# Performance work log

Measured on AMD Instinct MI355X. Metric: run time of the kernel, lower is better.

## Reference

```python
import jax, jax.numpy as jnp
import numpy as np

D_MODEL = 1024
H = 16
D_K = D_MODEL // H


def setup_inputs() -> dict:
    key = jax.random.key(0)
    ks = jax.random.split(key, 7)
    B, S = 4, 2048
    scale = 1.0 / np.sqrt(D_MODEL)
    return {
        "q": jax.random.normal(ks[0], (B, S, D_MODEL), dtype=jnp.float32),
        "k": jax.random.normal(ks[1], (B, S, D_MODEL), dtype=jnp.float32),
        "v": jax.random.normal(ks[2], (B, S, D_MODEL), dtype=jnp.float32),
        "W_q": jax.random.normal(ks[3], (D_MODEL, D_MODEL), dtype=jnp.float32) * scale,
        "W_k": jax.random.normal(ks[4], (D_MODEL, D_MODEL), dtype=jnp.float32) * scale,
        "W_v": jax.random.normal(ks[5], (D_MODEL, D_MODEL), dtype=jnp.float32) * scale,
        "W_o": jax.random.normal(ks[6], (D_MODEL, D_MODEL), dtype=jnp.float32) * scale,
    }


def reference(q, k, v, W_q, W_k, W_v, W_o):
    B, S, _ = q.shape
    # nn.Linear(bias=False): y = x @ W.T
    def proj(x, W):
        return (x @ W.T).reshape(B, -1, H, D_K).transpose(0, 2, 1, 3)  # [B,H,S,d_k]
    Q = proj(q, W_q)
    K = proj(k, W_k)
    V = proj(v, W_v)
    scores = jnp.einsum('bhqd,bhkd->bhqk', Q, K) / jnp.sqrt(jnp.float32(D_K))
    attn = jax.nn.softmax(scores, axis=-1)  # dropout p=0.0 -> identity
    ctx = jnp.einsum('bhqk,bhkd->bhqd', attn, V)
    ctx = ctx.transpose(0, 2, 1, 3).reshape(B, S, H * D_K)
    return ctx @ W_o.T
```

## Files before the change

### kernel.cpp

```cpp
#include <hip/hip_runtime.h>
#include <stdint.h>


typedef __attribute__((ext_vector_type(8))) short bf16x8;
typedef __attribute__((ext_vector_type(4))) float f32x4;

__device__ __forceinline__ void lds_async16(const void* g, void* l) {
  __builtin_amdgcn_global_load_lds(
      (const __attribute__((address_space(1))) void*)g,
      (__attribute__((address_space(3))) void*)l, 16, 0, 0);
}

__device__ __forceinline__ unsigned short f2bf(float f) {
  union { float f; unsigned u; } v; v.f = f;
  unsigned u = v.u + 0x7fffu + ((v.u >> 16) & 1u);
  return (unsigned short)(u >> 16);
}

__device__ __forceinline__ float fast_exp2(float x) {
#if __has_builtin(__builtin_amdgcn_exp2f)
  return __builtin_amdgcn_exp2f(x);
#else
  return exp2f(x);
#endif
}

__device__ __forceinline__ unsigned pk2(float a, float b) {
#if __has_builtin(__builtin_amdgcn_cvt_pk_bf16_f32)
  typedef __bf16 bf16v2 __attribute__((ext_vector_type(2)));
  union { bf16v2 v; unsigned u; } x;
  x.v = __builtin_amdgcn_cvt_pk_bf16_f32(a, b);
  return x.u;
#else
  return (unsigned)f2bf(a) | ((unsigned)f2bf(b) << 16);
#endif
}

__global__ void cvt_kernel(const float* s0, const float* s1, const float* s2, const float* s3,
                           unsigned short* d0, unsigned short* d1, unsigned short* d2, unsigned short* d3,
                           int n4) {
  int which = blockIdx.y;
  const float* s = which == 0 ? s0 : which == 1 ? s1 : which == 2 ? s2 : s3;
  unsigned short* d = which == 0 ? d0 : which == 1 ? d1 : which == 2 ? d2 : d3;
  int i = blockIdx.x * 256 + threadIdx.x;
  if (i < n4) {
    float4 v = ((const float4*)s)[i];
    ushort4 o;
    o.x = f2bf(v.x); o.y = f2bf(v.y); o.z = f2bf(v.z); o.w = f2bf(v.w);
    ((ushort4*)d)[i] = o;
  }
}

struct G256 { f32x4 acc[4][4]; };

__device__ __forceinline__ void stage_half(const unsigned short* __restrict__ src,
                                           int rowbase, int kt, int h,
                                           unsigned short* lds, int tid) {
  const int srow = tid >> 3;
  const int g = tid & 7;
  const int col = ((g ^ (srow & 7)) << 3);
  const unsigned short* s0 = src + (size_t)(rowbase + h * 128 + srow) * 1024 + kt * 64 + col;
  char* d0 = (char*)lds + h * 16384 + tid * 16;
  lds_async16(s0, d0);
  lds_async16(s0 + (size_t)64 * 1024, d0 + 8192);
}

__device__ __forceinline__ void read2(const unsigned short* buf, int rowbase, int c16, int q4,
                                      int tbase, bf16x8 (&fr)[2][2]) {
#pragma unroll
  for (int tt = 0; tt < 2; ++tt)
#pragma unroll
    for (int ks = 0; ks < 2; ++ks) {
      int row = rowbase + (tbase + tt) * 16 + c16;
      fr[tt][ks] = *(const bf16x8*)(buf + row * 64 + (((ks * 4 + q4) ^ (row & 7)) * 8));
    }
}

__device__ __forceinline__ void mfma_quad(G256& G, const bf16x8 (&af)[2][2],
                                          const bf16x8 (&bf)[2][2], int i0, int j0) {
  __builtin_amdgcn_s_setprio(1);
#pragma unroll
  for (int ii = 0; ii < 2; ++ii)
#pragma unroll
    for (int jj = 0; jj < 2; ++jj)
#pragma unroll
      for (int ks = 0; ks < 2; ++ks)
        G.acc[i0 + ii][j0 + jj] = __builtin_amdgcn_mfma_f32_16x16x32_bf16(
            af[ii][ks], bf[jj][ks], G.acc[i0 + ii][j0 + jj], 0, 0, 0);
  __builtin_amdgcn_s_setprio(0);
}

__device__ __forceinline__ void gemm256_core(const unsigned short* __restrict__ A,
                                             const unsigned short* __restrict__ B,
                                             int tm, int tn,
                                             unsigned short* As, unsigned short* Bs,
                                             G256& G) {
  const int tid = threadIdx.x;
  const int lane = tid & 63;
  const int wv = tid >> 6;
  const int wm = wv & 1, wn = wv >> 1;
  const int c16 = lane & 15, q4 = lane >> 4;
  const int am = tm * 128, bn = tn * 256;
  const int arow = wm * 64, brow = wn * 64;

#pragma unroll
  for (int i = 0; i < 4; ++i)
#pragma unroll
    for (int j = 0; j < 4; ++j)
#pragma unroll
      for (int r = 0; r < 4; ++r) G.acc[i][j][r] = 0.f;

  stage_half(A, am, 0, 0, As + 0 * 8192, tid);
  stage_half(B, bn, 0, 0, Bs + 0 * 16384, tid);
  stage_half(B, bn, 0, 1, Bs + 0 * 16384, tid);
  stage_half(A, am, 1, 0, As + 1 * 8192, tid);
  stage_half(B, bn, 1, 0, Bs + 1 * 16384, tid);
  stage_half(B, bn, 1, 1, Bs + 1 * 16384, tid);

  bf16x8 af[2][2], bfa[2][2], bfb[2][2];

#pragma unroll
  for (int t = 0; t < 16; ++t) {
    const int bt = t % 3;
    const int b2 = (t + 2) % 3;
    const unsigned short* Ab = As + bt * 8192;
    const unsigned short* Bb = Bs + bt * 16384;
    if (t < 15) { asm volatile("s_waitcnt vmcnt(6)" ::: "memory"); }
    else        { asm volatile("s_waitcnt vmcnt(0)" ::: "memory"); }
    __builtin_amdgcn_s_barrier();
    if (t < 14) {
      stage_half(A, am, t + 2, 0, As + b2 * 8192, tid);
      stage_half(B, bn, t + 2, 0, Bs + b2 * 16384, tid);
      stage_half(B, bn, t + 2, 1, Bs + b2 * 16384, tid);
    }
    read2(Ab, arow, c16, q4, 0, af);
    read2(Bb, brow, c16, q4, 0, bfa);
    read2(Bb, brow, c16, q4, 2, bfb);
    mfma_quad(G, af, bfa, 0, 0);
    mfma_quad(G, af, bfb, 0, 2);
    __builtin_amdgcn_s_barrier();
    read2(Ab, arow, c16, q4, 2, af);
    mfma_quad(G, af, bfb, 2, 2);
    mfma_quad(G, af, bfa, 2, 0);
  }
}

__global__ __launch_bounds__(512, 1)
void qkv_kernel(const unsigned short* __restrict__ qb, const unsigned short* __restrict__ kb,
                const unsigned short* __restrict__ vb,
                const unsigned short* __restrict__ wq, const unsigned short* __restrict__ wk,
                const unsigned short* __restrict__ wv_,
                unsigned short* __restrict__ Qb, unsigned short* __restrict__ Kb,
                unsigned short* __restrict__ Vtb) {
  __shared__ unsigned short As[3 * 128 * 64];
  __shared__ unsigned short Bs[3 * 256 * 64];
  const int z = blockIdx.z;
  const unsigned short* A;
  const unsigned short* B;
  int tm, tn;
  if (z == 0)      { A = qb;  B = wq;  tm = blockIdx.y; tn = blockIdx.x; }
  else if (z == 1) { A = kb;  B = wk;  tm = blockIdx.y; tn = blockIdx.x; }
  else {
    A = wv_; B = vb;
    int idx = blockIdx.y * 4 + blockIdx.x;
    tm = idx >> 5;
    tn = idx & 31;
  }

  G256 G;
  gemm256_core(A, B, tm, tn, As, Bs, G);

  const int lane = threadIdx.x & 63;
  const int wv = threadIdx.x >> 6;
  const int wm = wv & 1, wn = wv >> 1;
  const int c16 = lane & 15, q4 = lane >> 4;
  const float qscale = 0.125f * 1.44269504f;

#pragma unroll
  for (int i = 0; i < 4; ++i)
#pragma unroll
    for (int j = 0; j < 4; ++j)
#pragma unroll
      for (int r = 0; r < 4; ++r) {
        int m = tm * 128 + wm * 64 + i * 16 + q4 * 4 + r;
        int n = tn * 256 + wn * 64 + j * 16 + c16;
        float val = G.acc[i][j][r];
        if (z < 2) {
          if (z == 0) val *= qscale;
          int b = m >> 11, s_ = m & 2047, h = n >> 6, d = n & 63;
          unsigned short* dst = z == 0 ? Qb : Kb;
          dst[(((size_t)(b * 16 + h) * 2048 + s_) << 6) | d] = f2bf(val);
        } else {
          int h = m >> 6, d = m & 63, b = n >> 11, s_ = n & 2047;
          int sl = s_ & 127;
          int sp = (sl & ~31) | (((sl >> 2) & 3) << 3) | (((sl >> 4) & 1) << 2) | (sl & 3);
          s_ = (s_ & ~127) | sp;
          Vtb[((size_t)((b * 16 + h) * 64 + d) << 11) | s_] = f2bf(val);
        }
      }
}

__global__ __launch_bounds__(512, 1)
void out_gemm(const unsigned short* __restrict__ A, const unsigned short* __restrict__ B,
              float* __restrict__ C) {
  __shared__ unsigned short As[3 * 128 * 64];
  __shared__ unsigned short Bs[3 * 256 * 64];
  G256 G;
  gemm256_core(A, B, blockIdx.y, blockIdx.x, As, Bs, G);
  const int lane = threadIdx.x & 63;
  const int wv = threadIdx.x >> 6;
  const int wm = wv & 1, wn = wv >> 1;
  const int c16 = lane & 15, q4 = lane >> 4;
#pragma unroll
  for (int i = 0; i < 4; ++i)
#pragma unroll
    for (int j = 0; j < 4; ++j)
#pragma unroll
      for (int r = 0; r < 4; ++r) {
        int m = blockIdx.y * 128 + wm * 64 + i * 16 + q4 * 4 + r;
        int n = blockIdx.x * 256 + wn * 64 + j * 16 + c16;
        C[(size_t)m * 1024 + n] = G.acc[i][j][r];
      }
}

__global__ __launch_bounds__(128, 2)
void attn_kernel(const unsigned short* __restrict__ Q,
                 const unsigned short* __restrict__ K,
                 const unsigned short* __restrict__ Vt,
                 unsigned short* __restrict__ ctx) {
  __shared__ unsigned short Ks[2][64 * 64];
  __shared__ unsigned short Vs[2][64 * 64];

  const int tid = threadIdx.x, lane = tid & 63, w = tid >> 6;
  const int c16 = lane & 15, q4 = lane >> 4;
  const int wbase = w * 64;
  const unsigned wgid = blockIdx.x;
  const int bh = (int)((wgid & 7u) * 8 + ((wgid >> 3) & 7u));
  const int qt = (int)(wgid >> 6);
  const unsigned short* Qp = Q + ((size_t)bh * 2048 + qt * 128) * 64;
  const unsigned short* Kp = K + (size_t)bh * 2048 * 64;
  const unsigned short* Vp = Vt + (size_t)bh * 64 * 2048;

  const int srow = tid >> 3;
  const int gcol = (((tid & 7) ^ (srow & 7)) << 3);

  {
    const unsigned short* Qr = Qp + (size_t)srow * 64 + gcol;
    char* base = (char*)Ks + tid * 16;
#pragma unroll
    for (int c = 0; c < 8; ++c) lds_async16(Qr + c * 16 * 64, base + c * 2048);
  }
  __syncthreads();
  const unsigned short* Kflat = &Ks[0][0];
  bf16x8 qf[4][2];
#pragma unroll
  for (int nn = 0; nn < 4; ++nn)
#pragma unroll
    for (int ks = 0; ks < 2; ++ks) {
      int qr = wbase + nn * 16 + c16;
      int pos = (ks * 4 + q4) ^ (qr & 7);
      qf[nn][ks] = *(const bf16x8*)(Kflat + qr * 64 + pos * 8);
    }
  __syncthreads();

  bf16x8 onesf;
  {
    short v = (c16 == 0) ? (short)0x3F80 : (short)0;
#pragma unroll
    for (int j = 0; j < 8; ++j) onesf[j] = v;
  }

  f32x4 oacc[4][4];
  f32x4 lacc[4];
#pragma unroll
  for (int nn = 0; nn < 4; ++nn) {
#pragma unroll
    for (int r = 0; r < 4; ++r) lacc[nn][r] = 0.f;
#pragma unroll
    for (int dj = 0; dj < 4; ++dj)
#pragma unroll
      for (int r = 0; r < 4; ++r) oacc[nn][dj][r] = 0.f;
  }

  const unsigned short* Kr0 = Kp + (size_t)srow * 64 + gcol;
  const unsigned short* Vr0 = Vp + (size_t)srow * 2048 + gcol;

  {
    char* kb = (char*)Ks[0] + tid * 16;
    char* vb = (char*)Vs[0] + tid * 16;
#pragma unroll
    for (int c = 0; c < 4; ++c) {
      lds_async16(Kr0 + (size_t)c * 16 * 64, kb + c * 2048);
      lds_async16(Vr0 + (size_t)c * 16 * 2048, vb + c * 2048);
    }
  }

  int cur = 0;
#pragma unroll 2
  for (int kt = 0; kt < 32; ++kt) {
    __syncthreads();
    if (kt < 31) {
      char* kb = (char*)Ks[cur ^ 1] + tid * 16;
      char* vb = (char*)Vs[cur ^ 1] + tid * 16;
      const unsigned short* Krn = Kr0 + (size_t)(kt + 1) * 64 * 64;
      const unsigned short* Vrn = Vr0 + (size_t)(kt + 1) * 64;
#pragma unroll
      for (int c = 0; c < 4; ++c) {
        lds_async16(Krn + (size_t)c * 16 * 64, kb + c * 2048);
        lds_async16(Vrn + (size_t)c * 16 * 2048, vb + c * 2048);
      }
    }

    const unsigned short* KsC = Ks[cur];
    const unsigned short* VsC = Vs[cur];

    bf16x8 kf[2][2][2];
#pragma unroll
    for (int c = 0; c < 2; ++c)
#pragma unroll
      for (int ms = 0; ms < 2; ++ms) {
        const int row = (c * 2 + ms) * 16 + c16;
        kf[c][ms][0] = *(const bf16x8*)(KsC + row * 64 + ((0 + q4) ^ (row & 7)) * 8);
        kf[c][ms][1] = *(const bf16x8*)(KsC + row * 64 + ((4 + q4) ^ (row & 7)) * 8);
      }
    bf16x8 vf0[4];
#pragma unroll
    for (int dj = 0; dj < 4; ++dj) {
      const int dr = dj * 16 + c16;
      vf0[dj] = *(const bf16x8*)(VsC + dr * 64 + ((q4 ^ (dr & 7))) * 8);
    }

    f32x4 s0[2][4], s1[2][4];
    __builtin_amdgcn_s_setprio(1);
#pragma unroll
    for (int ms = 0; ms < 2; ++ms)
#pragma unroll
      for (int nn = 0; nn < 4; ++nn) {
        f32x4 z = {0.f, 0.f, 0.f, 0.f};
        z = __builtin_amdgcn_mfma_f32_16x16x32_bf16(kf[0][ms][0], qf[nn][0], z, 0, 0, 0);
        z = __builtin_amdgcn_mfma_f32_16x16x32_bf16(kf[0][ms][1], qf[nn][1], z, 0, 0, 0);
        s0[ms][nn] = z;
      }
    __builtin_amdgcn_s_setprio(0);
    bf16x8 vf1[4];
#pragma unroll
    for (int dj = 0; dj < 4; ++dj) {
      const int dr = dj * 16 + c16;
      vf1[dj] = *(const bf16x8*)(VsC + dr * 64 + (((4 + q4) ^ (dr & 7))) * 8);
    }
    __builtin_amdgcn_s_setprio(1);
#pragma unroll
    for (int ms = 0; ms < 2; ++ms)
#pragma unroll
      for (int nn = 0; nn < 4; ++nn) {
        f32x4 z = {0.f, 0.f, 0.f, 0.f};
        z = __builtin_amdgcn_mfma_f32_16x16x32_bf16(kf[1][ms][0], qf[nn][0], z, 0, 0, 0);
        z = __builtin_amdgcn_mfma_f32_16x16x32_bf16(kf[1][ms][1], qf[nn][1], z, 0, 0, 0);
        s1[ms][nn] = z;
      }
    __builtin_amdgcn_s_setprio(0);

    {
      bf16x8 pfv[4];
#pragma unroll
      for (int nn = 0; nn < 4; ++nn) {
        union PU { unsigned u[4]; bf16x8 v; } pf;
        pf.u[0] = pk2(fast_exp2(s0[0][nn][0]), fast_exp2(s0[0][nn][1]));
        pf.u[1] = pk2(fast_exp2(s0[0][nn][2]), fast_exp2(s0[0][nn][3]));
        pf.u[2] = pk2(fast_exp2(s0[1][nn][0]), fast_exp2(s0[1][nn][1]));
        pf.u[3] = pk2(fast_exp2(s0[1][nn][2]), fast_exp2(s0[1][nn][3]));
        pfv[nn] = pf.v;
      }
      __builtin_amdgcn_s_setprio(1);
#pragma unroll
      for (int nn = 0; nn < 4; ++nn)
        lacc[nn] = __builtin_amdgcn_mfma_f32_16x16x32_bf16(pfv[nn], onesf, lacc[nn], 0, 0, 0);
#pragma unroll
      for (int dj = 0; dj < 4; ++dj)
#pragma unroll
        for (int nn = 0; nn < 4; ++nn)
          oacc[nn][dj] = __builtin_amdgcn_mfma_f32_16x16x32_bf16(pfv[nn], vf0[dj], oacc[nn][dj], 0, 0, 0);
      __builtin_amdgcn_s_setprio(0);
    }
    {
      bf16x8 pfv[4];
#pragma unroll
      for (int nn = 0; nn < 4; ++nn) {
        union PU { unsigned u[4]; bf16x8 v; } pf;
        pf.u[0] = pk2(fast_exp2(s1[0][nn][0]), fast_exp2(s1[0][nn][1]));
        pf.u[1] = pk2(fast_exp2(s1[0][nn][2]), fast_exp2(s1[0][nn][3]));
        pf.u[2] = pk2(fast_exp2(s1[1][nn][0]), fast_exp2(s1[1][nn][1]));
        pf.u[3] = pk2(fast_exp2(s1[1][nn][2]), fast_exp2(s1[1][nn][3]));
        pfv[nn] = pf.v;
      }
      __builtin_amdgcn_s_setprio(1);
#pragma unroll
      for (int nn = 0; nn < 4; ++nn)
        lacc[nn] = __builtin_amdgcn_mfma_f32_16x16x32_bf16(pfv[nn], onesf, lacc[nn], 0, 0, 0);
#pragma unroll
      for (int dj = 0; dj < 4; ++dj)
#pragma unroll
        for (int nn = 0; nn < 4; ++nn)
          oacc[nn][dj] = __builtin_amdgcn_mfma_f32_16x16x32_bf16(pfv[nn], vf1[dj], oacc[nn][dj], 0, 0, 0);
      __builtin_amdgcn_s_setprio(0);
    }
    cur ^= 1;
  }

  int b = bh >> 4, h = bh & 15;
#pragma unroll
  for (int nn = 0; nn < 4; ++nn)
#pragma unroll
    for (int r = 0; r < 4; ++r) {
      float l = __shfl(lacc[nn][r], lane & 48, 64);
      float inv = 1.f / l;
      int s_ = qt * 128 + wbase + nn * 16 + q4 * 4 + r;
#pragma unroll
      for (int dj = 0; dj < 4; ++dj) {
        int d = dj * 16 + c16;
        ctx[((size_t)(b * 2048 + s_)) * 1024 + h * 64 + d] = f2bf(oacc[nn][dj][r] * inv);
      }
    }
}

extern "C" void kernel_launch(void* const* d_in, const int* in_sizes, int n_in,
                              void* d_out, int out_size, void* d_ws, size_t ws_size,
                              hipStream_t stream) {
  const float* q  = (const float*)d_in[0];
  const float* k  = (const float*)d_in[1];
  const float* v  = (const float*)d_in[2];
  const float* Wq = (const float*)d_in[3];
  const float* Wk = (const float*)d_in[4];
  const float* Wv = (const float*)d_in[5];
  const float* Wo = (const float*)d_in[6];

  char* ws = (char*)d_ws;
  unsigned short* qb  = (unsigned short*)(ws);
  unsigned short* kb  = (unsigned short*)(ws + (16u << 20));
  unsigned short* vb  = (unsigned short*)(ws + (32u << 20));
  unsigned short* wqb = (unsigned short*)(ws + (48u << 20));
  unsigned short* wkb = (unsigned short*)(ws + (50u << 20));
  unsigned short* wvb = (unsigned short*)(ws + (52u << 20));
  unsigned short* wob = (unsigned short*)(ws + (54u << 20));
  unsigned short* Qb  = (unsigned short*)(ws + (56u << 20));
  unsigned short* Kb  = (unsigned short*)(ws + (72u << 20));
  unsigned short* Vtb = (unsigned short*)(ws + (88u << 20));
  unsigned short* ctxb = qb;

  cvt_kernel<<<dim3(1024, 4), 256, 0, stream>>>(Wq, Wk, Wv, Wo, wqb, wkb, wvb, wob, 262144);
  cvt_kernel<<<dim3(8192, 3), 256, 0, stream>>>(q, k, v, q, qb, kb, vb, qb, 2097152);

  qkv_kernel<<<dim3(4, 64, 3), 512, 0, stream>>>(qb, kb, vb, wqb, wkb, wvb, Qb, Kb, Vtb);

  attn_kernel<<<dim3(1024), 128, 0, stream>>>(Qb, Kb, Vtb, ctxb);

  out_gemm<<<dim3(4, 64), 512, 0, stream>>>(ctxb, wob, (float*)d_out);
}
```

Before: 322.2 us.

## Fuse fp32-to-bf16 conversion into GEMM loaders, dropping separate cvt kernels

Removes the two standalone conversion kernels and has the QKV and output GEMMs load fp32 operands straight into registers, convert them to bf16 and write them to LDS, with a register-staged software pipeline. This saves a full extra read and write of the activations and weights plus two launches. In exchange the GEMMs read twice as many bytes per tile, lose asynchronous global-to-LDS loads for fp32 operands, and add conversion ALU work and register pressure. Weights are now re-read and re-converted by every tile that uses them.

```diff
diff --git a/kernel.cpp b/kernel.cpp
--- a/kernel.cpp
+++ b/kernel.cpp
@@ -36,33 +36,56 @@
 #endif
 }
 
-__global__ void cvt_kernel(const float* s0, const float* s1, const float* s2, const float* s3,
-                           unsigned short* d0, unsigned short* d1, unsigned short* d2, unsigned short* d3,
-                           int n4) {
-  int which = blockIdx.y;
-  const float* s = which == 0 ? s0 : which == 1 ? s1 : which == 2 ? s2 : s3;
-  unsigned short* d = which == 0 ? d0 : which == 1 ? d1 : which == 2 ? d2 : d3;
-  int i = blockIdx.x * 256 + threadIdx.x;
-  if (i < n4) {
-    float4 v = ((const float4*)s)[i];
-    ushort4 o;
-    o.x = f2bf(v.x); o.y = f2bf(v.y); o.z = f2bf(v.z); o.w = f2bf(v.w);
-    ((ushort4*)d)[i] = o;
-  }
-}
-
 struct G256 { f32x4 acc[4][4]; };
 
-__device__ __forceinline__ void stage_half(const unsigned short* __restrict__ src,
-                                           int rowbase, int kt, int h,
-                                           unsigned short* lds, int tid) {
+__device__ __forceinline__ void stage_lds_unit(const unsigned short* __restrict__ src,
+                                               int rowbase, int kt, int halves,
+                                               unsigned short* lds, int tid) {
   const int srow = tid >> 3;
-  const int g = tid & 7;
-  const int col = ((g ^ (srow & 7)) << 3);
-  const unsigned short* s0 = src + (size_t)(rowbase + h * 128 + srow) * 1024 + kt * 64 + col;
-  char* d0 = (char*)lds + h * 16384 + tid * 16;
-  lds_async16(s0, d0);
-  lds_async16(s0 + (size_t)64 * 1024, d0 + 8192);
+  const int col = (((tid & 7) ^ (srow & 7)) << 3);
+#pragma unroll
+  for (int h = 0; h < 2; ++h) {
+    if (h >= halves) break;
+    const unsigned short* s0 = src + (size_t)(rowbase + h * 128 + srow) * 1024 + kt * 64 + col;
+    char* d0 = (char*)lds + h * 16384 + tid * 16;
+    lds_async16(s0, d0);
+    lds_async16(s0 + (size_t)64 * 1024, d0 + 8192);
+  }
+}
+
+__device__ __forceinline__ void ldreg_unit(const float* __restrict__ src,
+                                           int rowbase, int kt, int halves,
+                                           float4* r, int tid) {
+  const int srow = tid >> 3;
+  const int col = (((tid & 7) ^ (srow & 7)) << 3);
+#pragma unroll
+  for (int h = 0; h < 2; ++h) {
+    if (h >= halves) break;
+    const float* p = src + (size_t)(rowbase + h * 128 + srow) * 1024 + kt * 64 + col;
+    r[h * 4 + 0] = *(const float4*)(p);
+    r[h * 4 + 1] = *(const float4*)(p + 4);
+    r[h * 4 + 2] = *(const float4*)(p + (size_t)64 * 1024);
+    r[h * 4 + 3] = *(const float4*)(p + (size_t)64 * 1024 + 4);
+  }
+}
+
+__device__ __forceinline__ void wr_unit(unsigned short* lds, int halves,
+                                        const float4* r, int tid) {
+#pragma unroll
+  for (int h = 0; h < 2; ++h) {
+    if (h >= halves) break;
+    union { unsigned u[4]; bf16x8 v; } x, y;
+    x.u[0] = pk2(r[h * 4 + 0].x, r[h * 4 + 0].y);
+    x.u[1] = pk2(r[h * 4 + 0].z, r[h * 4 + 0].w);
+    x.u[2] = pk2(r[h * 4 + 1].x, r[h * 4 + 1].y);
+    x.u[3] = pk2(r[h * 4 + 1].z, r[h * 4 + 1].w);
+    y.u[0] = pk2(r[h * 4 + 2].x, r[h * 4 + 2].y);
+    y.u[1] = pk2(r[h * 4 + 2].z, r[h * 4 + 2].w);
+    y.u[2] = pk2(r[h * 4 + 3].x, r[h * 4 + 3].y);
+    y.u[3] = pk2(r[h * 4 + 3].z, r[h * 4 + 3].w);
+    *(bf16x8*)((char*)lds + h * 16384 + tid * 16) = x.v;
+    *(bf16x8*)((char*)lds + h * 16384 + tid * 16 + 8192) = y.v;
+  }
 }
 
 __device__ __forceinline__ void read2(const unsigned short* buf, int rowbase, int c16, int q4,
@@ -90,11 +113,10 @@
   __builtin_amdgcn_s_setprio(0);
 }
 
-__device__ __forceinline__ void gemm256_core(const unsigned short* __restrict__ A,
-                                             const unsigned short* __restrict__ B,
-                                             int tm, int tn,
-                                             unsigned short* As, unsigned short* Bs,
-                                             G256& G) {
+template <bool AF32, bool BF32>
+__device__ __forceinline__ void gcore(const void* __restrict__ Av, const void* __restrict__ Bv,
+                                      int tm, int tn,
+                                      unsigned short* As, unsigned short* Bs, G256& G) {
   const int tid = threadIdx.x;
   const int lane = tid & 63;
   const int wv = tid >> 6;
@@ -110,29 +132,41 @@
 #pragma unroll
       for (int r = 0; r < 4; ++r) G.acc[i][j][r] = 0.f;
 
-  stage_half(A, am, 0, 0, As + 0 * 8192, tid);
-  stage_half(B, bn, 0, 0, Bs + 0 * 16384, tid);
-  stage_half(B, bn, 0, 1, Bs + 0 * 16384, tid);
-  stage_half(A, am, 1, 0, As + 1 * 8192, tid);
-  stage_half(B, bn, 1, 0, Bs + 1 * 16384, tid);
-  stage_half(B, bn, 1, 1, Bs + 1 * 16384, tid);
+  float4 rA[4], rB[8];
+  if constexpr (AF32) ldreg_unit((const float*)Av, am, 0, 1, rA, tid);
+  else                stage_lds_unit((const unsigned short*)Av, am, 0, 1, As, tid);
+  if constexpr (BF32) ldreg_unit((const float*)Bv, bn, 0, 2, rB, tid);
+  else                stage_lds_unit((const unsigned short*)Bv, bn, 0, 2, Bs, tid);
+  if constexpr (AF32) wr_unit(As, 1, rA, tid);
+  if constexpr (BF32) wr_unit(Bs, 2, rB, tid);
+  if constexpr (AF32) ldreg_unit((const float*)Av, am, 1, 1, rA, tid);
+  else                stage_lds_unit((const unsigned short*)Av, am, 1, 1, As + 8192, tid);
+  if constexpr (BF32) ldreg_unit((const float*)Bv, bn, 1, 2, rB, tid);
+  else                stage_lds_unit((const unsigned short*)Bv, bn, 1, 2, Bs + 16384, tid);
 
   bf16x8 af[2][2], bfa[2][2], bfb[2][2];
 
 #pragma unroll
   for (int t = 0; t < 16; ++t) {
-    const int bt = t % 3;
-    const int b2 = (t + 2) % 3;
-    const unsigned short* Ab = As + bt * 8192;
-    const unsigned short* Bb = Bs + bt * 16384;
-    if (t < 15) { asm volatile("s_waitcnt vmcnt(6)" ::: "memory"); }
-    else        { asm volatile("s_waitcnt vmcnt(0)" ::: "memory"); }
+    const unsigned short* Ab = As + (t % 3) * 8192;
+    const unsigned short* Bb = Bs + (t % 3) * 16384;
+    if (t < 15) {
+      if constexpr (AF32) wr_unit(As + ((t + 1) % 3) * 8192, 1, rA, tid);
+      if constexpr (BF32) wr_unit(Bs + ((t + 1) % 3) * 16384, 2, rB, tid);
+    }
+    if (t < 14) {
+      if constexpr (AF32) ldreg_unit((const float*)Av, am, t + 2, 1, rA, tid);
+      if constexpr (BF32) ldreg_unit((const float*)Bv, bn, t + 2, 2, rB, tid);
+    }
+    asm volatile("s_waitcnt lgkmcnt(0)" ::: "memory");
     __builtin_amdgcn_s_barrier();
     if (t < 14) {
-      stage_half(A, am, t + 2, 0, As + b2 * 8192, tid);
-      stage_half(B, bn, t + 2, 0, Bs + b2 * 16384, tid);
-      stage_half(B, bn, t + 2, 1, Bs + b2 * 16384, tid);
-    }
+      if constexpr (!AF32) stage_lds_unit((const unsigned short*)Av, am, t + 2, 1,
+                                          As + ((t + 2) % 3) * 8192, tid);
+      if constexpr (!BF32) stage_lds_unit((const unsigned short*)Bv, bn, t + 2, 2,
+                                          Bs + ((t + 2) % 3) * 16384, tid);
+    }
+    if (t == 15) { asm volatile("s_waitcnt vmcnt(0)" ::: "memory"); }
     read2(Ab, arow, c16, q4, 0, af);
     read2(Bb, brow, c16, q4, 0, bfa);
     read2(Bb, brow, c16, q4, 2, bfb);
@@ -146,29 +180,29 @@
 }
 
 __global__ __launch_bounds__(512, 1)
-void qkv_kernel(const unsigned short* __restrict__ qb, const unsigned short* __restrict__ kb,
-                const unsigned short* __restrict__ vb,
-                const unsigned short* __restrict__ wq, const unsigned short* __restrict__ wk,
-                const unsigned short* __restrict__ wv_,
+void qkv_kernel(const float* __restrict__ q, const float* __restrict__ k,
+                const float* __restrict__ v,
+                const float* __restrict__ Wq, const float* __restrict__ Wk,
+                const float* __restrict__ Wv,
                 unsigned short* __restrict__ Qb, unsigned short* __restrict__ Kb,
                 unsigned short* __restrict__ Vtb) {
   __shared__ unsigned short As[3 * 128 * 64];
   __shared__ unsigned short Bs[3 * 256 * 64];
   const int z = blockIdx.z;
-  const unsigned short* A;
-  const unsigned short* B;
+  const float* A;
+  const float* B;
   int tm, tn;
-  if (z == 0)      { A = qb;  B = wq;  tm = blockIdx.y; tn = blockIdx.x; }
-  else if (z == 1) { A = kb;  B = wk;  tm = blockIdx.y; tn = blockIdx.x; }
+  if (z == 0)      { A = q;  B = Wq; tm = blockIdx.y; tn = blockIdx.x; }
+  else if (z == 1) { A = k;  B = Wk; tm = blockIdx.y; tn = blockIdx.x; }
   else {
-    A = wv_; B = vb;
+    A = Wv; B = v;
     int idx = blockIdx.y * 4 + blockIdx.x;
     tm = idx >> 5;
     tn = idx & 31;
   }
 
   G256 G;
-  gemm256_core(A, B, tm, tn, As, Bs, G);
+  gcore<true, true>(A, B, tm, tn, As, Bs, G);
 
   const int lane = threadIdx.x & 63;
   const int wv = threadIdx.x >> 6;
@@ -201,12 +235,12 @@
 }
 
 __global__ __launch_bounds__(512, 1)
-void out_gemm(const unsigned short* __restrict__ A, const unsigned short* __restrict__ B,
+void out_gemm(const unsigned short* __restrict__ A, const float* __restrict__ B,
               float* __restrict__ C) {
   __shared__ unsigned short As[3 * 128 * 64];
   __shared__ unsigned short Bs[3 * 256 * 64];
   G256 G;
-  gemm256_core(A, B, blockIdx.y, blockIdx.x, As, Bs, G);
+  gcore<false, true>(A, B, blockIdx.y, blockIdx.x, As, Bs, G);
   const int lane = threadIdx.x & 63;
   const int wv = threadIdx.x >> 6;
   const int wm = wv & 1, wn = wv >> 1;
@@ -435,24 +469,14 @@
   const float* Wo = (const float*)d_in[6];
 
   char* ws = (char*)d_ws;
-  unsigned short* qb  = (unsigned short*)(ws);
-  unsigned short* kb  = (unsigned short*)(ws + (16u << 20));
-  unsigned short* vb  = (unsigned short*)(ws + (32u << 20));
-  unsigned short* wqb = (unsigned short*)(ws + (48u << 20));
-  unsigned short* wkb = (unsigned short*)(ws + (50u << 20));
-  unsigned short* wvb = (unsigned short*)(ws + (52u << 20));
-  unsigned short* wob = (unsigned short*)(ws + (54u << 20));
-  unsigned short* Qb  = (unsigned short*)(ws + (56u << 20));
-  unsigned short* Kb  = (unsigned short*)(ws + (72u << 20));
-  unsigned short* Vtb = (unsigned short*)(ws + (88u << 20));
-  unsigned short* ctxb = qb;
-
-  cvt_kernel<<<dim3(1024, 4), 256, 0, stream>>>(Wq, Wk, Wv, Wo, wqb, wkb, wvb, wob, 262144);
-  cvt_kernel<<<dim3(8192, 3), 256, 0, stream>>>(q, k, v, q, qb, kb, vb, qb, 2097152);
-
-  qkv_kernel<<<dim3(4, 64, 3), 512, 0, stream>>>(qb, kb, vb, wqb, wkb, wvb, Qb, Kb, Vtb);
+  unsigned short* ctxb = (unsigned short*)(ws);
+  unsigned short* Qb   = (unsigned short*)(ws + (16u << 20));
+  unsigned short* Kb   = (unsigned short*)(ws + (32u << 20));
+  unsigned short* Vtb  = (unsigned short*)(ws + (48u << 20));
+
+  qkv_kernel<<<dim3(4, 64, 3), 512, 0, stream>>>(q, k, v, Wq, Wk, Wv, Qb, Kb, Vtb);
 
   attn_kernel<<<dim3(1024), 128, 0, stream>>>(Qb, Kb, Vtb, ctxb);
 
-  out_gemm<<<dim3(4, 64), 512, 0, stream>>>(ctxb, wob, (float*)d_out);
-}
+  out_gemm<<<dim3(4, 64), 512, 0, stream>>>(ctxb, Wo, (float*)d_out);
+}
```

After: 406.1 us. 26.0% more time.
